# Kernel tuning notes

Measured on AMD Instinct MI355X. Metric: run time of the kernel, lower is better.

Reference implementation:

```python
import jax, jax.numpy as jnp
import numpy as np

B, N, KNB, F, H = 1, 50000, 16, 128, 128
BN_EPS = 1e-3  # keras BatchNormalization default epsilon
ALPHA = 0.3    # keras LeakyReLU default negative slope


def setup_inputs() -> dict:
    key = jax.random.key(0)
    ks = jax.random.split(key, 14)
    s_in = 1.0 / np.sqrt(F)
    s_cat = 1.0 / np.sqrt(F + H)
    return {
        'embeddings': jax.random.normal(ks[0], (B, N, F), jnp.float32),
        'weights': jnp.zeros((1, 1), jnp.float32),  # unused in call_att
        'neighbor_set': jax.random.randint(ks[1], (B, N, KNB), 0, N),
        'Wq': jax.random.normal(ks[2], (F, H), jnp.float32) * s_in,
        'bq': jnp.zeros((H,), jnp.float32),
        'Wk': jax.random.normal(ks[3], (F, H), jnp.float32) * s_in,
        'bk': jnp.zeros((H,), jnp.float32),
        'Wv': jax.random.normal(ks[4], (F, H), jnp.float32) * s_in,
        'bv': jnp.zeros((H,), jnp.float32),
        'W1': jax.random.normal(ks[5], (F + H, H), jnp.float32) * s_cat,
        'b1': jnp.zeros((H,), jnp.float32),
        'gamma': 1.0 + 0.1 * jax.random.normal(ks[6], (H,), jnp.float32),
        'beta': 0.1 * jax.random.normal(ks[7], (H,), jnp.float32),
        'mov_mean': 0.1 * jax.random.normal(ks[8], (H,), jnp.float32),
        'mov_var': 1.0 + 0.1 * jax.random.uniform(ks[9], (H,), jnp.float32),
    }


def reference(embeddings, weights, neighbor_set, Wq, bq, Wk, bk, Wv, bv,
              W1, b1, gamma, beta, mov_mean, mov_var):
    lrelu = lambda x: jax.nn.leaky_relu(x, ALPHA)
    # batched gather: nb[b, n, k] = embeddings[b, neighbor_set[b, n, k]]  -> [B,N,K,F]
    nb = jax.vmap(lambda e, idx: e[idx])(embeddings, neighbor_set)
    q = lrelu(embeddings @ Wq + bq)      # [B,N,H]
    k = lrelu(nb @ Wk + bk)              # [B,N,K,H]
    v = lrelu(nb @ Wv + bv)              # [B,N,K,H]
    # Q is tiled across the K neighbor rows in the original; every attention row
    # is identical, so mean-pool over rows == single-query attention. Same math.
    scores = jnp.einsum('bnh,bnkh->bnk', q, k)          # dot-product, no scale
    attn = jax.nn.softmax(scores, axis=-1)
    pooled = jnp.einsum('bnk,bnkh->bnh', attn, v)       # [B,N,H]
    h = lrelu(jnp.concatenate([embeddings, pooled], axis=-1) @ W1 + b1)
    h = h / (jnp.linalg.norm(h, axis=2, keepdims=True) + 1e-6)
    # BatchNormalization (inference form, axis=-1)
    return gamma * (h - mov_mean) * jax.lax.rsqrt(mov_var + BN_EPS) + beta
```

## Files before the change

kernel.cpp:

```cpp
#include <hip/hip_runtime.h>
#include <hip/hip_bf16.h>

#define N_NODES 50000
#define KNB 16
#define FDIM 128
#define HDIM 128
#define ALPHA 0.3f
#define BN_EPS 1e-3f

typedef __bf16 v8bf __attribute__((ext_vector_type(8)));
typedef float v4f __attribute__((ext_vector_type(4)));

__device__ __forceinline__ float bf2f(unsigned int u16bits) {
    union { float f; unsigned int i; } x;
    x.i = u16bits << 16;
    return x.f;
}

__device__ __forceinline__ unsigned short f2bf(float f) {
    union { float f; unsigned int u; } x;
    x.f = f;
    unsigned int r = x.u + 0x7fffu + ((x.u >> 16) & 1u);
    return (unsigned short)(r >> 16);
}

__device__ __forceinline__ float lrelu(float x) { return x > 0.f ? x : ALPHA * x; }

__device__ __forceinline__ v8bf load8f(const float* p) {
    float4 a = *(const float4*)p;
    float4 b = *(const float4*)(p + 4);
    union { v8bf v; unsigned short u[8]; } r;
    r.u[0] = f2bf(a.x); r.u[1] = f2bf(a.y); r.u[2] = f2bf(a.z); r.u[3] = f2bf(a.w);
    r.u[4] = f2bf(b.x); r.u[5] = f2bf(b.y); r.u[6] = f2bf(b.z); r.u[7] = f2bf(b.w);
    return r.v;
}

__global__ __launch_bounds__(256) void qkv_kernel(
    const float* __restrict__ E,
    const float* __restrict__ Wq, const float* __restrict__ bq,
    const float* __restrict__ Wk, const float* __restrict__ bk,
    const float* __restrict__ Wv, const float* __restrict__ bv,
    float* __restrict__ Qo, unsigned short* __restrict__ Ko,
    unsigned short* __restrict__ Vo)
{
    __shared__ unsigned short sW[128 * 136];

    const int tid  = threadIdx.x;
    const int wave = tid >> 6;
    const int lane = tid & 63;
    const int quad = lane >> 4;
    const int j    = lane & 15;
    const int row0 = blockIdx.x * 128 + wave * 32;

    const float* Ws[3] = {Wq, Wk, Wv};
    const float* bs[3] = {bq, bk, bv};

    const int ar0 = min(row0 + j,      N_NODES - 1);
    const int ar1 = min(row0 + 16 + j, N_NODES - 1);

    for (int w = 0; w < 3; ++w) {
        const float* W = Ws[w];
        for (int idx = tid; idx < 128 * 128; idx += 256) {
            int k = idx >> 7, n = idx & 127;
            sW[n * 136 + k] = f2bf(W[idx]);
        }
        __syncthreads();

        v4f acc[2][8];
#pragma unroll
        for (int rb = 0; rb < 2; ++rb)
#pragma unroll
            for (int c = 0; c < 8; ++c) acc[rb][c] = (v4f){0.f, 0.f, 0.f, 0.f};

#pragma unroll
        for (int ks = 0; ks < 4; ++ks) {
            const int k0 = ks * 32 + quad * 8;
            v8bf a0 = load8f(E + (size_t)ar0 * FDIM + k0);
            v8bf a1 = load8f(E + (size_t)ar1 * FDIM + k0);
            v8bf b[8];
#pragma unroll
            for (int c = 0; c < 8; ++c)
                b[c] = *(const v8bf*)(&sW[(c * 16 + j) * 136 + k0]);
#pragma unroll
            for (int c = 0; c < 8; ++c) {
                acc[0][c] = __builtin_amdgcn_mfma_f32_16x16x32_bf16(a0, b[c], acc[0][c], 0, 0, 0);
                acc[1][c] = __builtin_amdgcn_mfma_f32_16x16x32_bf16(a1, b[c], acc[1][c], 0, 0, 0);
            }
        }

        const float* bias = bs[w];
#pragma unroll
        for (int c = 0; c < 8; ++c) {
            const int col = c * 16 + j;
            const float bv_ = bias[col];
#pragma unroll
            for (int rb = 0; rb < 2; ++rb) {
#pragma unroll
                for (int i = 0; i < 4; ++i) {
                    const int r = row0 + rb * 16 + quad * 4 + i;
                    if (r < N_NODES) {
                        const float x = lrelu(acc[rb][c][i] + bv_);
                        if (w == 0)      Qo[(size_t)r * HDIM + col] = x;
                        else if (w == 1) Ko[(size_t)r * HDIM + col] = f2bf(x);
                        else             Vo[(size_t)r * HDIM + col] = f2bf(x);
                    }
                }
            }
        }
        __syncthreads();
    }
}

__global__ __launch_bounds__(256) void attn_kernel(
    float* __restrict__ QP, const unsigned short* __restrict__ K,
    const unsigned short* __restrict__ V, const int* __restrict__ nbr,
    int n_nodes)
{
    const int tid  = threadIdx.x;
    const int wave = tid >> 6;
    const int lane = tid & 63;
    const int node = blockIdx.x * 4 + wave;
    if (node >= n_nodes) return;

    const float2 qp = ((const float2*)(QP + (size_t)node * HDIM))[lane];

    int idxs[KNB];
    const int* nb = nbr + node * KNB;
#pragma unroll
    for (int t = 0; t < KNB; ++t) {
        int id = nb[t];
        idxs[t] = ((unsigned)id < (unsigned)n_nodes) ? id : 0;
    }

    float sc[KNB];
#pragma unroll
    for (int t = 0; t < KNB; ++t) {
        const unsigned int kp = ((const unsigned int*)(K + (size_t)idxs[t] * HDIM))[lane];
        float p = qp.x * bf2f(kp & 0xffffu) + qp.y * bf2f(kp >> 16);
#pragma unroll
        for (int off = 32; off >= 1; off >>= 1) p += __shfl_xor(p, off, 64);
        sc[t] = p;
    }

    float m = sc[0];
#pragma unroll
    for (int t = 1; t < KNB; ++t) m = fmaxf(m, sc[t]);
    float s = 0.f;
#pragma unroll
    for (int t = 0; t < KNB; ++t) { sc[t] = __expf(sc[t] - m); s += sc[t]; }
    const float inv = 1.f / s;

    float p0 = 0.f, p1 = 0.f;
#pragma unroll
    for (int t = 0; t < KNB; ++t) {
        const unsigned int vp = ((const unsigned int*)(V + (size_t)idxs[t] * HDIM))[lane];
        const float a = sc[t] * inv;
        p0 += a * bf2f(vp & 0xffffu);
        p1 += a * bf2f(vp >> 16);
    }

    ((float2*)(QP + (size_t)node * HDIM))[lane] = make_float2(p0, p1);
}

__global__ __launch_bounds__(256) void out_kernel(
    const float* __restrict__ E, const float* __restrict__ W1,
    const float* __restrict__ b1,
    const float* __restrict__ gamma, const float* __restrict__ beta,
    const float* __restrict__ mmean, const float* __restrict__ mvar,
    float* __restrict__ OutP)
{
    __shared__ unsigned short sW[128 * 136];

    const int tid  = threadIdx.x;
    const int wave = tid >> 6;
    const int lane = tid & 63;
    const int quad = lane >> 4;
    const int j    = lane & 15;
    const int row0 = blockIdx.x * 128 + wave * 32;

    const int ar0 = min(row0 + j,      N_NODES - 1);
    const int ar1 = min(row0 + 16 + j, N_NODES - 1);

    v4f acc[2][8];
#pragma unroll
    for (int rb = 0; rb < 2; ++rb)
#pragma unroll
        for (int c = 0; c < 8; ++c) acc[rb][c] = (v4f){0.f, 0.f, 0.f, 0.f};

    for (int half = 0; half < 2; ++half) {
        for (int idx = tid; idx < 128 * 128; idx += 256) {
            int k = idx >> 7, n = idx & 127;
            sW[n * 136 + k] = f2bf(W1[idx + half * 16384]);
        }
        __syncthreads();

        const float* Abase = (half == 0) ? E : (const float*)OutP;
#pragma unroll
        for (int ks = 0; ks < 4; ++ks) {
            const int k0 = ks * 32 + quad * 8;
            v8bf a0 = load8f(Abase + (size_t)ar0 * 128 + k0);
            v8bf a1 = load8f(Abase + (size_t)ar1 * 128 + k0);
            v8bf b[8];
#pragma unroll
            for (int c = 0; c < 8; ++c)
                b[c] = *(const v8bf*)(&sW[(c * 16 + j) * 136 + k0]);
#pragma unroll
            for (int c = 0; c < 8; ++c) {
                acc[0][c] = __builtin_amdgcn_mfma_f32_16x16x32_bf16(a0, b[c], acc[0][c], 0, 0, 0);
                acc[1][c] = __builtin_amdgcn_mfma_f32_16x16x32_bf16(a1, b[c], acc[1][c], 0, 0, 0);
            }
        }
        __syncthreads();
    }

    float scale_[8], shift_[8], bias_[8];
#pragma unroll
    for (int c = 0; c < 8; ++c) {
        const int col = c * 16 + j;
        const float g  = gamma[col];
        const float be = beta[col];
        const float mu = mmean[col];
        const float vv = mvar[col];
        const float s = g * rsqrtf(vv + BN_EPS);
        scale_[c] = s;
        shift_[c] = be - mu * s;
        bias_[c]  = b1[col];
    }

#pragma unroll
    for (int rb = 0; rb < 2; ++rb)
#pragma unroll
        for (int c = 0; c < 8; ++c)
#pragma unroll
            for (int i = 0; i < 4; ++i)
                acc[rb][c][i] = lrelu(acc[rb][c][i] + bias_[c]);

#pragma unroll
    for (int rb = 0; rb < 2; ++rb) {
#pragma unroll
        for (int i = 0; i < 4; ++i) {
            float ss = 0.f;
#pragma unroll
            for (int c = 0; c < 8; ++c) ss += acc[rb][c][i] * acc[rb][c][i];
            ss += __shfl_xor(ss, 1, 64);
            ss += __shfl_xor(ss, 2, 64);
            ss += __shfl_xor(ss, 4, 64);
            ss += __shfl_xor(ss, 8, 64);
            const float invn = 1.f / (sqrtf(ss) + 1e-6f);
            const int r = row0 + rb * 16 + quad * 4 + i;
            if (r < N_NODES) {
#pragma unroll
                for (int c = 0; c < 8; ++c) {
                    const float o = acc[rb][c][i] * invn * scale_[c] + shift_[c];
                    OutP[(size_t)r * HDIM + c * 16 + j] = o;
                }
            }
        }
    }
}

extern "C" void kernel_launch(void* const* d_in, const int* in_sizes, int n_in,
                              void* d_out, int out_size, void* d_ws, size_t ws_size,
                              hipStream_t stream)
{
    const float* E     = (const float*)d_in[0];
    const int*   nbr   = (const int*)d_in[2];
    const float* Wq    = (const float*)d_in[3];
    const float* bq    = (const float*)d_in[4];
    const float* Wk    = (const float*)d_in[5];
    const float* bk    = (const float*)d_in[6];
    const float* Wv    = (const float*)d_in[7];
    const float* bv    = (const float*)d_in[8];
    const float* W1    = (const float*)d_in[9];
    const float* b1    = (const float*)d_in[10];
    const float* gam   = (const float*)d_in[11];
    const float* bet   = (const float*)d_in[12];
    const float* mmean = (const float*)d_in[13];
    const float* mvar  = (const float*)d_in[14];

    unsigned short* Ko = (unsigned short*)d_ws;
    unsigned short* Vo = Ko + (size_t)N_NODES * HDIM;
    float* QP = (float*)d_out;

    const int gridA = (N_NODES + 127) / 128;
    qkv_kernel<<<gridA, 256, 0, stream>>>(E, Wq, bq, Wk, bk, Wv, bv, QP, Ko, Vo);
    attn_kernel<<<(N_NODES + 3) / 4, 256, 0, stream>>>(QP, Ko, Vo, nbr, N_NODES);
    out_kernel<<<gridA, 256, 0, stream>>>(E, W1, b1, gam, bet, mmean, mvar, QP);
}
```

Before: 223.6 us.

## Pre-transpose bf16 weights, interleave K/V, and restructure attention gather

Adds a prep kernel that converts all weights to bf16 and transposes them once, so the GEMM kernels copy them into shared memory with 16-byte vector loads instead of converting and transposing per block. The qkv kernel loads embedding fragments once and reuses them for all three projections. K and V are interleaved per node, and the attention kernel computes all 16 scores in parallel with four lanes per neighbor, using a shared-memory exchange in place of serial wave-wide reductions. The extra launch and the block-level barrier in attention add some overhead, and the attention grid now assumes the node count is divisible by four.

```diff
diff --git a/kernel.cpp b/kernel.cpp
--- a/kernel.cpp
+++ b/kernel.cpp
@@ -10,11 +10,13 @@
 
 typedef __bf16 v8bf __attribute__((ext_vector_type(8)));
 typedef float v4f __attribute__((ext_vector_type(4)));
-
-__device__ __forceinline__ float bf2f(unsigned int u16bits) {
-    union { float f; unsigned int i; } x;
-    x.i = u16bits << 16;
-    return x.f;
+typedef unsigned short ushort_t;
+
+__device__ __forceinline__ float blo(unsigned int u) {
+    union { float f; unsigned int i; } x; x.i = u << 16; return x.f;
+}
+__device__ __forceinline__ float bhi(unsigned int u) {
+    union { float f; unsigned int i; } x; x.i = u & 0xffff0000u; return x.f;
 }
 
 __device__ __forceinline__ unsigned short f2bf(float f) {
@@ -24,26 +26,50 @@
     return (unsigned short)(r >> 16);
 }
 
+__device__ __forceinline__ unsigned int pk2(float a, float b) {
+    __hip_bfloat162 h = __float22bfloat162_rn(make_float2(a, b));
+    union { __hip_bfloat162 h; unsigned int u; } r; r.h = h; return r.u;
+}
+
 __device__ __forceinline__ float lrelu(float x) { return x > 0.f ? x : ALPHA * x; }
 
 __device__ __forceinline__ v8bf load8f(const float* p) {
-    float4 a = *(const float4*)p;
-    float4 b = *(const float4*)(p + 4);
-    union { v8bf v; unsigned short u[8]; } r;
-    r.u[0] = f2bf(a.x); r.u[1] = f2bf(a.y); r.u[2] = f2bf(a.z); r.u[3] = f2bf(a.w);
-    r.u[4] = f2bf(b.x); r.u[5] = f2bf(b.y); r.u[6] = f2bf(b.z); r.u[7] = f2bf(b.w);
+    float4 A = ((const float4*)p)[0];
+    float4 B = ((const float4*)p)[1];
+    union { v8bf v; unsigned int u[4]; } r;
+    r.u[0] = pk2(A.x, A.y); r.u[1] = pk2(A.z, A.w);
+    r.u[2] = pk2(B.x, B.y); r.u[3] = pk2(B.z, B.w);
     return r.v;
 }
 
+__global__ __launch_bounds__(256) void prep_kernel(
+    const float* __restrict__ Wq, const float* __restrict__ Wk,
+    const float* __restrict__ Wv, const float* __restrict__ W1,
+    ushort_t* __restrict__ WT)
+{
+    const int idx = blockIdx.x * 256 + threadIdx.x;
+    if (idx < 16384) {
+        int k = idx >> 7, n = idx & 127;
+        WT[n * 128 + k] = f2bf(Wq[idx]);
+    } else if (idx < 32768) {
+        int i = idx - 16384; int k = i >> 7, n = i & 127;
+        WT[16384 + n * 128 + k] = f2bf(Wk[i]);
+    } else if (idx < 49152) {
+        int i = idx - 32768; int k = i >> 7, n = i & 127;
+        WT[32768 + n * 128 + k] = f2bf(Wv[i]);
+    } else if (idx < 81920) {
+        int i = idx - 49152; int k = i >> 7, n = i & 127;
+        WT[49152 + n * 256 + k] = f2bf(W1[i]);
+    }
+}
+
 __global__ __launch_bounds__(256) void qkv_kernel(
-    const float* __restrict__ E,
-    const float* __restrict__ Wq, const float* __restrict__ bq,
-    const float* __restrict__ Wk, const float* __restrict__ bk,
-    const float* __restrict__ Wv, const float* __restrict__ bv,
-    float* __restrict__ Qo, unsigned short* __restrict__ Ko,
-    unsigned short* __restrict__ Vo)
-{
-    __shared__ unsigned short sW[128 * 136];
+    const float* __restrict__ E, const ushort_t* __restrict__ WT,
+    const float* __restrict__ bq, const float* __restrict__ bk,
+    const float* __restrict__ bv,
+    float* __restrict__ Qo, ushort_t* __restrict__ KV)
+{
+    __shared__ ushort_t sW[128 * 136];
 
     const int tid  = threadIdx.x;
     const int wave = tid >> 6;
@@ -52,17 +78,24 @@
     const int j    = lane & 15;
     const int row0 = blockIdx.x * 128 + wave * 32;
 
-    const float* Ws[3] = {Wq, Wk, Wv};
-    const float* bs[3] = {bq, bk, bv};
-
     const int ar0 = min(row0 + j,      N_NODES - 1);
     const int ar1 = min(row0 + 16 + j, N_NODES - 1);
 
+    v8bf a0f[4], a1f[4];
+#pragma unroll
+    for (int ks = 0; ks < 4; ++ks) {
+        const int k0 = ks * 32 + quad * 8;
+        a0f[ks] = load8f(E + (size_t)ar0 * FDIM + k0);
+        a1f[ks] = load8f(E + (size_t)ar1 * FDIM + k0);
+    }
+
+    const float* biases[3] = {bq, bk, bv};
+
     for (int w = 0; w < 3; ++w) {
-        const float* W = Ws[w];
-        for (int idx = tid; idx < 128 * 128; idx += 256) {
-            int k = idx >> 7, n = idx & 127;
-            sW[n * 136 + k] = f2bf(W[idx]);
+        const ushort_t* Wsrc = WT + w * 16384;
+        for (int i = tid; i < 2048; i += 256) {
+            int n = i >> 4, kc = i & 15;
+            *(uint4*)(&sW[n * 136 + kc * 8]) = *(const uint4*)(Wsrc + n * 128 + kc * 8);
         }
         __syncthreads();
 
@@ -75,20 +108,18 @@
 #pragma unroll
         for (int ks = 0; ks < 4; ++ks) {
             const int k0 = ks * 32 + quad * 8;
-            v8bf a0 = load8f(E + (size_t)ar0 * FDIM + k0);
-            v8bf a1 = load8f(E + (size_t)ar1 * FDIM + k0);
             v8bf b[8];
 #pragma unroll
             for (int c = 0; c < 8; ++c)
                 b[c] = *(const v8bf*)(&sW[(c * 16 + j) * 136 + k0]);
 #pragma unroll
             for (int c = 0; c < 8; ++c) {
-                acc[0][c] = __builtin_amdgcn_mfma_f32_16x16x32_bf16(a0, b[c], acc[0][c], 0, 0, 0);
-                acc[1][c] = __builtin_amdgcn_mfma_f32_16x16x32_bf16(a1, b[c], acc[1][c], 0, 0, 0);
+                acc[0][c] = __builtin_amdgcn_mfma_f32_16x16x32_bf16(a0f[ks], b[c], acc[0][c], 0, 0, 0);
+                acc[1][c] = __builtin_amdgcn_mfma_f32_16x16x32_bf16(a1f[ks], b[c], acc[1][c], 0, 0, 0);
             }
         }
 
-        const float* bias = bs[w];
+        const float* bias = biases[w];
 #pragma unroll
         for (int c = 0; c < 8; ++c) {
             const int col = c * 16 + j;
@@ -101,8 +132,8 @@
                     if (r < N_NODES) {
                         const float x = lrelu(acc[rb][c][i] + bv_);
                         if (w == 0)      Qo[(size_t)r * HDIM + col] = x;
-                        else if (w == 1) Ko[(size_t)r * HDIM + col] = f2bf(x);
-                        else             Vo[(size_t)r * HDIM + col] = f2bf(x);
+                        else if (w == 1) KV[(size_t)r * 256 + col] = f2bf(x);
+                        else             KV[(size_t)r * 256 + 128 + col] = f2bf(x);
                     }
                 }
             }
@@ -112,64 +143,84 @@
 }
 
 __global__ __launch_bounds__(256) void attn_kernel(
-    float* __restrict__ QP, const unsigned short* __restrict__ K,
-    const unsigned short* __restrict__ V, const int* __restrict__ nbr,
-    int n_nodes)
-{
+    float* __restrict__ QP, const ushort_t* __restrict__ KV,
+    const int* __restrict__ nbr)
+{
+    __shared__ float sE[4 * 16];
+
     const int tid  = threadIdx.x;
     const int wave = tid >> 6;
     const int lane = tid & 63;
-    const int node = blockIdx.x * 4 + wave;
-    if (node >= n_nodes) return;
-
-    const float2 qp = ((const float2*)(QP + (size_t)node * HDIM))[lane];
-
-    int idxs[KNB];
+    const int node = __builtin_amdgcn_readfirstlane(blockIdx.x * 4 + wave);
+
+    const int t = lane >> 2;
+    const int s = lane & 3;
+
     const int* nb = nbr + node * KNB;
-#pragma unroll
-    for (int t = 0; t < KNB; ++t) {
-        int id = nb[t];
-        idxs[t] = ((unsigned)id < (unsigned)n_nodes) ? id : 0;
-    }
-
-    float sc[KNB];
-#pragma unroll
-    for (int t = 0; t < KNB; ++t) {
-        const unsigned int kp = ((const unsigned int*)(K + (size_t)idxs[t] * HDIM))[lane];
-        float p = qp.x * bf2f(kp & 0xffffu) + qp.y * bf2f(kp >> 16);
-#pragma unroll
-        for (int off = 32; off >= 1; off >>= 1) p += __shfl_xor(p, off, 64);
-        sc[t] = p;
-    }
-
-    float m = sc[0];
-#pragma unroll
-    for (int t = 1; t < KNB; ++t) m = fmaxf(m, sc[t]);
-    float s = 0.f;
-#pragma unroll
-    for (int t = 0; t < KNB; ++t) { sc[t] = __expf(sc[t] - m); s += sc[t]; }
-    const float inv = 1.f / s;
+    int idt = nb[t];
+    idt = ((unsigned)idt < (unsigned)N_NODES) ? idt : 0;
+
+    const uint4* kbase = (const uint4*)(KV + (size_t)idt * 256 + s * 32);
+    uint4 kk[4];
+#pragma unroll
+    for (int i = 0; i < 4; ++i) kk[i] = kbase[i];
+
+    const float4* qbase = (const float4*)(QP + (size_t)node * HDIM + s * 32);
+    float4 qv[8];
+#pragma unroll
+    for (int i = 0; i < 8; ++i) qv[i] = qbase[i];
+
+    float p = 0.f;
+#pragma unroll
+    for (int i = 0; i < 4; ++i) {
+        const float4 qa = qv[2 * i], qb = qv[2 * i + 1];
+        p += qa.x * blo(kk[i].x) + qa.y * bhi(kk[i].x)
+           + qa.z * blo(kk[i].y) + qa.w * bhi(kk[i].y)
+           + qb.x * blo(kk[i].z) + qb.y * bhi(kk[i].z)
+           + qb.z * blo(kk[i].w) + qb.w * bhi(kk[i].w);
+    }
+    p += __shfl_xor(p, 1, 64);
+    p += __shfl_xor(p, 2, 64);
+
+    float m = p;
+    m = fmaxf(m, __shfl_xor(m, 4, 64));
+    m = fmaxf(m, __shfl_xor(m, 8, 64));
+    m = fmaxf(m, __shfl_xor(m, 16, 64));
+    m = fmaxf(m, __shfl_xor(m, 32, 64));
+
+    const float e = __expf(p - m);
+    if (s == 0) sE[wave * 16 + t] = e;
+    __syncthreads();
+
+    float ear[16];
+#pragma unroll
+    for (int i = 0; i < 4; ++i)
+        ((float4*)ear)[i] = ((const float4*)(sE + wave * 16))[i];
+    float sum = 0.f;
+#pragma unroll
+    for (int tt = 0; tt < KNB; ++tt) sum += ear[tt];
+    const float inv = 1.f / sum;
 
     float p0 = 0.f, p1 = 0.f;
 #pragma unroll
-    for (int t = 0; t < KNB; ++t) {
-        const unsigned int vp = ((const unsigned int*)(V + (size_t)idxs[t] * HDIM))[lane];
-        const float a = sc[t] * inv;
-        p0 += a * bf2f(vp & 0xffffu);
-        p1 += a * bf2f(vp >> 16);
-    }
-
-    ((float2*)(QP + (size_t)node * HDIM))[lane] = make_float2(p0, p1);
+    for (int tt = 0; tt < KNB; ++tt) {
+        int id = nb[tt];
+        id = ((unsigned)id < (unsigned)N_NODES) ? id : 0;
+        const unsigned int vp = *(const unsigned int*)(KV + (size_t)id * 256 + 128 + 2 * lane);
+        p0 += ear[tt] * blo(vp);
+        p1 += ear[tt] * bhi(vp);
+    }
+    ((float2*)(QP + (size_t)node * HDIM))[lane] = make_float2(p0 * inv, p1 * inv);
 }
 
 __global__ __launch_bounds__(256) void out_kernel(
-    const float* __restrict__ E, const float* __restrict__ W1,
+    const float* __restrict__ E, const ushort_t* __restrict__ W1T,
     const float* __restrict__ b1,
     const float* __restrict__ gamma, const float* __restrict__ beta,
     const float* __restrict__ mmean, const float* __restrict__ mvar,
     float* __restrict__ OutP)
 {
-    __shared__ unsigned short sW[128 * 136];
+    __shared__ ushort_t sW[128 * 136];
 
     const int tid  = threadIdx.x;
     const int wave = tid >> 6;
@@ -188,9 +239,10 @@
         for (int c = 0; c < 8; ++c) acc[rb][c] = (v4f){0.f, 0.f, 0.f, 0.f};
 
     for (int half = 0; half < 2; ++half) {
-        for (int idx = tid; idx < 128 * 128; idx += 256) {
-            int k = idx >> 7, n = idx & 127;
-            sW[n * 136 + k] = f2bf(W1[idx + half * 16384]);
+        for (int i = tid; i < 2048; i += 256) {
+            int n = i >> 4, kc = i & 15;
+            *(uint4*)(&sW[n * 136 + kc * 8]) =
+                *(const uint4*)(W1T + n * 256 + half * 128 + kc * 8);
         }
         __syncthreads();
 
@@ -217,13 +269,9 @@
 #pragma unroll
     for (int c = 0; c < 8; ++c) {
         const int col = c * 16 + j;
-        const float g  = gamma[col];
-        const float be = beta[col];
-        const float mu = mmean[col];
-        const float vv = mvar[col];
-        const float s = g * rsqrtf(vv + BN_EPS);
-        scale_[c] = s;
-        shift_[c] = be - mu * s;
+        const float sc = gamma[col] * rsqrtf(mvar[col] + BN_EPS);
+        scale_[c] = sc;
+        shift_[c] = beta[col] - mmean[col] * sc;
         bias_[c]  = b1[col];
     }
 
@@ -251,8 +299,8 @@
             if (r < N_NODES) {
 #pragma unroll
                 for (int c = 0; c < 8; ++c) {
-                    const float o = acc[rb][c][i] * invn * scale_[c] + shift_[c];
-                    OutP[(size_t)r * HDIM + c * 16 + j] = o;
+                    OutP[(size_t)r * HDIM + c * 16 + j] =
+                        acc[rb][c][i] * invn * scale_[c] + shift_[c];
                 }
             }
         }
@@ -278,12 +326,13 @@
     const float* mmean = (const float*)d_in[13];
     const float* mvar  = (const float*)d_in[14];
 
-    unsigned short* Ko = (unsigned short*)d_ws;
-    unsigned short* Vo = Ko + (size_t)N_NODES * HDIM;
+    ushort_t* KV = (ushort_t*)d_ws;
+    ushort_t* WT = KV + (size_t)N_NODES * 256;
     float* QP = (float*)d_out;
 
     const int gridA = (N_NODES + 127) / 128;
-    qkv_kernel<<<gridA, 256, 0, stream>>>(E, Wq, bq, Wk, bk, Wv, bv, QP, Ko, Vo);
-    attn_kernel<<<(N_NODES + 3) / 4, 256, 0, stream>>>(QP, Ko, Vo, nbr, N_NODES);
-    out_kernel<<<gridA, 256, 0, stream>>>(E, W1, b1, gam, bet, mmean, mvar, QP);
-}
+    prep_kernel<<<320, 256, 0, stream>>>(Wq, Wk, Wv, W1, WT);
+    qkv_kernel<<<gridA, 256, 0, stream>>>(E, WT, bq, bk, bv, QP, KV);
+    attn_kernel<<<N_NODES / 4, 256, 0, stream>>>(QP, KV, nbr);
+    out_kernel<<<gridA, 256, 0, stream>>>(E, WT + 49152, b1, gam, bet, mmean, mvar, QP);
+}
```

After: 229.9 us. 1.03x slower.
